# Optimization experiments

Measured on AMD Instinct MI355X. Metric: run time of the kernel, lower is better.

Reference implementation:

```python
import jax, jax.numpy as jnp
import numpy as np

B, P, F, H, NF, E, V, L = 128, 196, 2048, 512, 512, 512, 10000, 20
T = L - 1
EPS = 1e-5  # BatchNorm eps (eval mode, running_mean=0, running_var=1)


def setup_inputs() -> dict:
    key = jax.random.key(0)
    ks = jax.random.split(key, 16)

    def kaiming(k, out_d, in_d):
        return jax.random.normal(k, (out_d, in_d), jnp.float32) * np.float32(np.sqrt(2.0 / in_d))

    encoder_feat = jax.random.normal(ks[0], (B, P, F), jnp.float32)
    gt_captions = jax.random.randint(ks[1], (B, L), 0, V)
    # lengths in [2, L], sorted descending (torch code assumes this), max forced to L
    captions_len = jnp.sort(jax.random.randint(ks[2], (B,), 2, L + 1))[::-1].at[0].set(L)

    emb = jax.random.uniform(ks[3], (V, E), jnp.float32, -0.1, 0.1)
    Wfa = kaiming(ks[4], NF, F); bfa = jnp.zeros((NF,), jnp.float32)
    Wha = kaiming(ks[5], NF, H); bha = jnp.zeros((NF,), jnp.float32)
    Wv = kaiming(ks[6], 1, NF); bv = jnp.zeros((1,), jnp.float32)
    Wh0 = kaiming(ks[7], H, F); bh0 = jnp.zeros((H,), jnp.float32)
    Wc0 = kaiming(ks[8], H, F); bc0 = jnp.zeros((H,), jnp.float32)
    gamma_h = jnp.ones((H,), jnp.float32); beta_h = jnp.zeros((H,), jnp.float32)
    gamma_c = jnp.ones((H,), jnp.float32); beta_c = jnp.zeros((H,), jnp.float32)
    Wfb = kaiming(ks[9], F, H); bfb = jnp.zeros((F,), jnp.float32)
    s = np.float32(1.0 / np.sqrt(H))  # torch LSTMCell default init range
    Wih = jax.random.uniform(ks[10], (4 * H, E + F), jnp.float32, -s, s)
    Whh = jax.random.uniform(ks[11], (4 * H, H), jnp.float32, -s, s)
    bih = jax.random.uniform(ks[12], (4 * H,), jnp.float32, -s, s)
    bhh = jax.random.uniform(ks[13], (4 * H,), jnp.float32, -s, s)
    Wfc = kaiming(ks[14], V, H); bfc = jnp.zeros((V,), jnp.float32)

    return dict(encoder_feat=encoder_feat, emb=emb, Wfa=Wfa, bfa=bfa, Wha=Wha, bha=bha,
                Wv=Wv, bv=bv, Wh0=Wh0, bh0=bh0, Wc0=Wc0, bc0=bc0,
                gamma_h=gamma_h, beta_h=beta_h, gamma_c=gamma_c, beta_c=beta_c,
                Wfb=Wfb, bfb=bfb, Wih=Wih, Whh=Whh, bih=bih, bhh=bhh,
                Wfc=Wfc, bfc=bfc, gt_captions=gt_captions, captions_len=captions_len)


def reference(encoder_feat, emb, Wfa, bfa, Wha, bha, Wv, bv, Wh0, bh0, Wc0, bc0,
              gamma_h, beta_h, gamma_c, beta_c, Wfb, bfb, Wih, Whh, bih, bhh,
              Wfc, bfc, gt_captions, captions_len):
    # Eval-mode semantics: dropout = identity, weight-drop inactive,
    # BatchNorm1d uses default running stats (mean=0, var=1).
    def bn(x, g, b):
        return g * (x / jnp.sqrt(1.0 + EPS)) + b

    feat = encoder_feat.mean(axis=1)                       # [B, F]
    h = bn(jax.nn.sigmoid(feat @ Wh0.T + bh0), gamma_h, beta_h)
    c = bn(jax.nn.sigmoid(feat @ Wc0.T + bc0), gamma_c, beta_c)

    # attention key projection is h-independent: hoist out of the time loop
    feat_att = jnp.einsum('bpf,nf->bpn', encoder_feat, Wfa) + bfa  # [B, P, NF]
    emb_seq = emb[gt_captions]                                      # [B, L, E]

    # ragged batch handled by masking (equivalent to torch's [:batch_size_t] slicing)
    mask = (jnp.arange(T)[:, None] < (captions_len - 1)[None, :]).astype(encoder_feat.dtype)  # [T, B]
    xs = (jnp.swapaxes(emb_seq[:, :T], 0, 1), mask)

    def step(carry, xt):
        h, c = carry
        emb_t, m = xt                                      # [B, E], [B]
        att = jax.nn.relu(feat_att + (h @ Wha.T + bha)[:, None, :])
        e = jnp.einsum('bpn,n->bp', att, Wv[0]) + bv[0]    # [B, P]
        alpha = jax.nn.softmax(e, axis=1)
        context = jnp.einsum('bpf,bp->bf', encoder_feat, alpha)
        gate = jax.nn.sigmoid(h @ Wfb.T + bfb)             # [B, F]
        x = jnp.concatenate([emb_t, gate * context], axis=1)
        gates = x @ Wih.T + bih + h @ Whh.T + bhh          # [B, 4H]
        i, f, g, o = jnp.split(gates, 4, axis=1)
        c_new = jax.nn.sigmoid(f) * c + jax.nn.sigmoid(i) * jnp.tanh(g)
        h_new = jax.nn.sigmoid(o) * jnp.tanh(c_new)
        preds = h_new @ Wfc.T + bfc                        # [B, V]
        mf = m[:, None]
        return (h_new, c_new), (preds * mf, alpha * mf)

    _, (preds, alphas) = jax.lax.scan(step, (h, c), xs)
    predictions = jnp.swapaxes(preds, 0, 1)                # [B, T, V]
    alphas = jnp.swapaxes(alphas, 0, 1)                    # [B, T, P]
    return predictions, alphas
```

## Files before the change

kernel.cpp:

```cpp
#include <hip/hip_runtime.h>
#include <cstdint>
#include <cstddef>

#define B_  128
#define P_  196
#define F_  2048
#define H_  512
#define NF_ 512
#define E_  512
#define V_  10000
#define L_  20
#define T_  19
#define NPAD_ 10112

typedef short s8v __attribute__((ext_vector_type(8)));
typedef float f32x4 __attribute__((ext_vector_type(4)));
typedef unsigned short u16x8 __attribute__((ext_vector_type(8)));

__device__ __forceinline__ float sigf(float x) { return 1.0f / (1.0f + expf(-x)); }
__device__ __forceinline__ ushort f2b(float f) {
    unsigned u = __builtin_bit_cast(unsigned, f);
    u += 0x7fff + ((u >> 16) & 1);
    return (ushort)(u >> 16);
}
__device__ __forceinline__ float b2f(ushort h) {
    unsigned u = ((unsigned)h) << 16;
    return __builtin_bit_cast(float, u);
}

__global__ __launch_bounds__(256)
void zero_buf(float4* __restrict__ p, int n16) {
    int i = blockIdx.x * 256 + threadIdx.x;
    if (i < n16) p[i] = make_float4(0.f, 0.f, 0.f, 0.f);
}

__global__ __launch_bounds__(256)
void cast_mat(const float* __restrict__ s, ushort* __restrict__ d,
              long long total, int cols, int sld, int srows) {
    long long i4 = ((long long)blockIdx.x * 256 + threadIdx.x) * 4;
    if (i4 >= total) return;
    int n = (int)(i4 / cols);
    int k = (int)(i4 - (long long)n * cols);
    float4 v = make_float4(0.f, 0.f, 0.f, 0.f);
    if (n < srows) v = *(const float4*)(s + (size_t)n * sld + k);
    ushort4 o;
    o.x = f2b(v.x); o.y = f2b(v.y); o.z = f2b(v.z); o.w = f2b(v.w);
    *(ushort4*)(d + i4) = o;
}

__global__ __launch_bounds__(256)
void cast_perm(const float* __restrict__ s, ushort* __restrict__ d,
               int cols, int sld) {
    int idx = blockIdx.x * 256 + threadIdx.x;
    int i4 = idx * 4;
    int n = i4 / cols;
    int k = i4 - n * cols;
    int r = (n & 3) * H_ + (n >> 2);
    float4 v = *(const float4*)(s + (size_t)r * sld + k);
    ushort4 o;
    o.x = f2b(v.x); o.y = f2b(v.y); o.z = f2b(v.z); o.w = f2b(v.w);
    *(ushort4*)(d + (size_t)n * cols + k) = o;
}

__global__ __launch_bounds__(256)
void build_bg(const float* __restrict__ bih, const float* __restrict__ bhh,
              float* __restrict__ bg) {
    int n = blockIdx.x * 256 + threadIdx.x;
    int r = (n & 3) * H_ + (n >> 2);
    bg[n] = bih[r] + bhh[r];
}

#define NCP_ (2560 + NPAD_)
__global__ __launch_bounds__(256)
void build_bcp(const float* __restrict__ bha, const float* __restrict__ bfb,
               const float* __restrict__ bfc, float* __restrict__ bcp) {
    int n = blockIdx.x * 256 + threadIdx.x;
    if (n >= NCP_) return;
    float v;
    if (n < 512) v = bha[n];
    else if (n < 2560) v = bfb[n - 512];
    else { int r = n - 2560; v = (r < V_) ? bfc[r] : 0.0f; }
    bcp[n] = v;
}

__global__ __launch_bounds__(256)
void mean_cast_kernel(const float* __restrict__ enc, ushort* __restrict__ encb,
                      float* __restrict__ feat) {
    int b = blockIdx.x >> 3;
    int f = ((blockIdx.x & 7) << 8) + threadIdx.x;
    const float* p = enc + (size_t)b * P_ * F_ + f;
    ushort* pb = encb + (size_t)b * P_ * F_ + f;
    float s = 0.0f;
    for (int q = 0; q < P_; q++) {
        float v = p[(size_t)q * F_];
        pb[(size_t)q * F_] = f2b(v);
        s += v;
    }
    feat[b * F_ + f] = s * (1.0f / 196.0f);
}

__global__ __launch_bounds__(256) void mean_kernel(const float* __restrict__ enc,
                                                   float* __restrict__ feat) {
    int b = blockIdx.x >> 3;
    int f = ((blockIdx.x & 7) << 8) + threadIdx.x;
    const float* p = enc + (size_t)b * P_ * F_ + f;
    float s = 0.0f;
    for (int q = 0; q < P_; q++) s += p[(size_t)q * F_];
    feat[b * F_ + f] = s * (1.0f / 196.0f);
}

__global__ __launch_bounds__(256) void gather_b(const float* __restrict__ emb,
                                                const int* __restrict__ gt,
                                                ushort* __restrict__ embx) {
    int idx = blockIdx.x * 256 + threadIdx.x;
    int i4 = idx * 4;
    int e = i4 & (E_ - 1);
    int bt = i4 >> 9;
    int b = bt / T_, t = bt - b * T_;
    int tok = gt[b * L_ + t];
    float4 v = *(const float4*)(emb + (size_t)tok * E_ + e);
    ushort4 o;
    o.x = f2b(v.x); o.y = f2b(v.y); o.z = f2b(v.z); o.w = f2b(v.w);
    *(ushort4*)(embx + i4) = o;
}

__global__ __launch_bounds__(256)
void gemm_biasb(const float* __restrict__ A, int lda,
                const float* __restrict__ W, int ldw,
                const float* __restrict__ bias,
                ushort* __restrict__ C, long long ldc,
                int M, int N, int K) {
    __shared__ float As[16][65];
    __shared__ float Ws[16][65];
    const int tid = threadIdx.x;
    const int m0 = blockIdx.y << 6;
    const int n0 = blockIdx.x << 6;
    const int row = tid >> 2;
    const int kq  = (tid & 3) << 2;
    const int ty = tid >> 4, tx = tid & 15;
    float acc[4][4] = {};
    for (int k0 = 0; k0 < K; k0 += 16) {
        float4 av = make_float4(0.f, 0.f, 0.f, 0.f);
        float4 wv = make_float4(0.f, 0.f, 0.f, 0.f);
        int m = m0 + row;
        if (m < M) av = *(const float4*)(A + (size_t)m * lda + k0 + kq);
        int n = n0 + row;
        if (n < N) wv = *(const float4*)(W + (size_t)n * ldw + k0 + kq);
        __syncthreads();
        As[kq + 0][row] = av.x; As[kq + 1][row] = av.y;
        As[kq + 2][row] = av.z; As[kq + 3][row] = av.w;
        Ws[kq + 0][row] = wv.x; Ws[kq + 1][row] = wv.y;
        Ws[kq + 2][row] = wv.z; Ws[kq + 3][row] = wv.w;
        __syncthreads();
#pragma unroll
        for (int k = 0; k < 16; k++) {
            float a[4], w[4];
#pragma unroll
            for (int i = 0; i < 4; i++) a[i] = As[k][(ty << 2) + i];
#pragma unroll
            for (int j = 0; j < 4; j++) w[j] = Ws[k][(tx << 2) + j];
#pragma unroll
            for (int i = 0; i < 4; i++)
#pragma unroll
                for (int j = 0; j < 4; j++)
                    acc[i][j] = fmaf(a[i], w[j], acc[i][j]);
        }
    }
#pragma unroll
    for (int i = 0; i < 4; i++) {
        int m = m0 + (ty << 2) + i;
        if (m >= M) continue;
#pragma unroll
        for (int j = 0; j < 4; j++) {
            int n = n0 + (tx << 2) + j;
            if (n >= N) continue;
            C[(size_t)m * ldc + n] = f2b(acc[i][j] + bias[n]);
        }
    }
}

enum { MEPI_NONE = 0, MEPI_BIAS = 1, MEPI_BIASB = 2, MEPI_PREDS = 3 };

__device__ __forceinline__ void stage_tile(const ushort* __restrict__ g, int ld,
                                           int row0, int k0, ushort* lds,
                                           int rows, int w, int l) {
    int nchunk = rows >> 4;
    for (int c = w; c < nchunk; c += 4) {
        int flat = c * 1024 + l * 16;
        int r = flat >> 6;
        int ce = (flat & 63) >> 1;
        const ushort* gp = g + (size_t)(row0 + r) * ld + (k0 + ce);
        __builtin_amdgcn_global_load_lds(
            (const __attribute__((address_space(1))) void*)gp,
            (__attribute__((address_space(3))) void*)(lds + c * 512),
            16, 0, 0);
    }
}

template <int BM, int EPI, int DUAL, int SWZ = 0, int MSK = 0>
__global__ __launch_bounds__(256)
void mfma_gemm(const ushort* __restrict__ A1, int lda1,
               const ushort* __restrict__ W1, int ldw1, int K1,
               const ushort* __restrict__ A2, int lda2,
               const ushort* __restrict__ W2, int ldw2, int K2,
               const float* __restrict__ bias, void* __restrict__ Cout, long long ldc,
               void* __restrict__ Cout2,
               int M, int N,
               const int* __restrict__ clen, int tcur) {
    __shared__ ushort As[BM * 32];
    __shared__ ushort Bs[128 * 32];
    const int tid = threadIdx.x;
    const int w = tid >> 6, l = tid & 63;
    const int wr = w >> 1, wc = w & 1;
    constexpr int WM = BM / 2;
    constexpr int AF = WM / 16;
    int bx = blockIdx.x, by = blockIdx.y;
    if (SWZ) {
        const int gx = gridDim.x;
        const int nwg = gx * gridDim.y;
        const int fid = by * gx + bx;
        const int q = nwg >> 3, r = nwg & 7;
        const int xcd = fid & 7, idx = fid >> 3;
        const int nf = (xcd < r ? xcd * (q + 1)
                                : r * (q + 1) + (xcd - r) * q) + idx;
        bx = nf % gx; by = nf / gx;
    }
    if (MSK) {
        int cl = clen[by * BM + (l & (BM - 1))];
        if (!__any(tcur < cl - 1)) return;
    }
    const int m0 = by * BM;
    const int n0 = bx * 128;
    const int lrow = l & 15, lk8 = (l >> 4) * 8;
    const int kz = blockIdx.z, nzz = gridDim.z;

    f32x4 acc[AF][4] = {};

    for (int pass = 0; pass < 1 + DUAL; pass++) {
        const ushort* A = pass ? A2 : A1;
        const ushort* W = pass ? W2 : W1;
        const int lda = pass ? lda2 : lda1;
        const int ldw = pass ? ldw2 : ldw1;
        const int K  = pass ? K2 : K1;
        const int chunk = K / nzz;
        const int kbeg = kz * chunk;
        const int kend = kbeg + chunk;
        for (int k0 = kbeg; k0 < kend; k0 += 32) {
            __syncthreads();
            stage_tile(A, lda, m0, k0, As, BM, w, l);
            stage_tile(W, ldw, n0, k0, Bs, 128, w, l);
            __syncthreads();
            s8v af[AF], bf[4];
#pragma unroll
            for (int i = 0; i < AF; i++)
                af[i] = *(const s8v*)(As + (wr * WM + i * 16 + lrow) * 32 + lk8);
#pragma unroll
            for (int j = 0; j < 4; j++)
                bf[j] = *(const s8v*)(Bs + (wc * 64 + j * 16 + lrow) * 32 + lk8);
#pragma unroll
            for (int i = 0; i < AF; i++)
#pragma unroll
                for (int j = 0; j < 4; j++)
                    acc[i][j] = __builtin_amdgcn_mfma_f32_16x16x32_bf16(
                        af[i], bf[j], acc[i][j], 0, 0, 0);
        }
    }

    float* Cz = (float*)Cout + (size_t)kz * (size_t)M * ldc;
#pragma unroll
    for (int i = 0; i < AF; i++) {
        int rb = m0 + wr * WM + i * 16 + (l >> 4) * 4;
#pragma unroll
        for (int j = 0; j < 4; j++) {
            int n = n0 + wc * 64 + j * 16 + (l & 15);
            if (n >= N) continue;
#pragma unroll
            for (int r = 0; r < 4; r++) {
                int m = rb + r;
                float v = acc[i][j][r];
                if (EPI == MEPI_NONE) {
                    Cz[(size_t)m * ldc + n] = v;
                } else if (EPI == MEPI_BIAS) {
                    ((float*)Cout)[(size_t)m * ldc + n] = v + bias[n];
                } else if (EPI == MEPI_BIASB) {
                    ((ushort*)Cout)[(size_t)m * ldc + n] = f2b(v + bias[n]);
                } else if (EPI == MEPI_PREDS) {
                    if (n < V_) {
                        int bb = m & (B_ - 1);
                        int tt = m >> 7;
                        float mk = (tt < clen[bb] - 1) ? 1.0f : 0.0f;
                        ((float*)Cout)[((size_t)bb * T_ + tt) * (size_t)V_ + n] =
                            (v + bias[n]) * mk;
                    }
                }
            }
        }
    }
}

__global__ __launch_bounds__(256)
void h0c0_final(const float* __restrict__ part,
                const float* __restrict__ b0,
                const float* __restrict__ g0,
                const float* __restrict__ bt0,
                float* __restrict__ cbuf, ushort* __restrict__ hb) {
    int idx = blockIdx.x * 256 + threadIdx.x;
    int b = idx >> 9, j = idx & 511;
    const float rbn = 1.0f / sqrtf(1.0f + 1e-5f);
    float sh = b0[j], sc = b0[j + 512];
    for (int z = 0; z < 4; z++) {
        sh += part[((size_t)z * B_ + b) * 1024 + j];
        sc += part[((size_t)z * B_ + b) * 1024 + j + 512];
    }
    float hv = g0[j] * (sigf(sh) * rbn) + bt0[j];
    float cv = g0[j + 512] * (sigf(sc) * rbn) + bt0[j + 512];
    cbuf[idx] = cv;
    hb[idx] = f2b(hv);
}

template <int BF>
__global__ __launch_bounds__(256)
void attn_ctx(const void* __restrict__ encv, const ushort* __restrict__ fa,
              const float* __restrict__ combo, const float* __restrict__ Wv,
              float* __restrict__ alphas_out, const int* __restrict__ clen,
              ushort* __restrict__ gctxb, int t) {
    int b = blockIdx.x >> 1;
    if (t >= clen[b] - 1) return;
    int half = blockIdx.x & 1;
    int tid = threadIdx.x;
    int w = tid >> 6, l = tid & 63;
    __shared__ float eS[256];
    __shared__ float red[256];
    __shared__ float pc[128 * 8];
    const float* hap = combo + (size_t)b * 2560;
    float ha8[8], wv8[8];
#pragma unroll
    for (int i = 0; i < 8; i++) { ha8[i] = hap[l * 8 + i]; wv8[i] = Wv[l * 8 + i]; }
    eS[tid] = -1e30f;
    __syncthreads();
    const ushort* fab = fa + (size_t)b * P_ * NF_;
    for (int p = w; p < P_; p += 4) {
        const ushort* fp = fab + (size_t)p * NF_ + l * 8;
        ushort4 u0 = *(const ushort4*)fp;
        ushort4 u1 = *(const ushort4*)(fp + 4);
        float s = 0.0f, v;
        v = b2f(u0.x) + ha8[0]; v = v > 0.f ? v : 0.f; s = fmaf(v, wv8[0], s);
        v = b2f(u0.y) + ha8[1]; v = v > 0.f ? v : 0.f; s = fmaf(v, wv8[1], s);
        v = b2f(u0.z) + ha8[2]; v = v > 0.f ? v : 0.f; s = fmaf(v, wv8[2], s);
        v = b2f(u0.w) + ha8[3]; v = v > 0.f ? v : 0.f; s = fmaf(v, wv8[3], s);
        v = b2f(u1.x) + ha8[4]; v = v > 0.f ? v : 0.f; s = fmaf(v, wv8[4], s);
        v = b2f(u1.y) + ha8[5]; v = v > 0.f ? v : 0.f; s = fmaf(v, wv8[5], s);
        v = b2f(u1.z) + ha8[6]; v = v > 0.f ? v : 0.f; s = fmaf(v, wv8[6], s);
        v = b2f(u1.w) + ha8[7]; v = v > 0.f ? v : 0.f; s = fmaf(v, wv8[7], s);
#pragma unroll
        for (int off = 32; off > 0; off >>= 1) s += __shfl_down(s, off, 64);
        if (l == 0) eS[p] = s;
    }
    __syncthreads();
    float ev = eS[tid];
    red[tid] = ev;
    __syncthreads();
    for (int s = 128; s > 0; s >>= 1) {
        if (tid < s) red[tid] = fmaxf(red[tid], red[tid + s]);
        __syncthreads();
    }
    float mx = red[0];
    __syncthreads();
    float ex = expf(ev - mx);
    red[tid] = ex;
    __syncthreads();
    for (int s = 128; s > 0; s >>= 1) {
        if (tid < s) red[tid] += red[tid + s];
        __syncthreads();
    }
    float inv = 1.0f / red[0];
    float a = ex * inv;
    __syncthreads();
    eS[tid] = a;
    if (half == 0 && tid < P_) {
        alphas_out[((size_t)b * T_ + t) * P_ + tid] = a;
    }
    __syncthreads();

    int tl = tid & 127;
    int pr = tid >> 7;
    int pp0 = pr * 98;
    int f0 = (half << 10) + tl * 8;
    float s[8] = {};
    if (BF) {
        const ushort* ep = (const ushort*)encv + (size_t)b * P_ * F_ +
                           (size_t)pp0 * F_ + f0;
        for (int p = 0; p < 98; p++) {
            u16x8 u = *(const u16x8*)(ep + (size_t)p * F_);
            float al = eS[pp0 + p];
#pragma unroll
            for (int i = 0; i < 8; i++) s[i] = fmaf(al, b2f(u[i]), s[i]);
        }
    } else {
        const float* ep = (const float*)encv + (size_t)b * P_ * F_ +
                          (size_t)pp0 * F_ + f0;
        for (int p = 0; p < 98; p++) {
            float4 u0 = *(const float4*)(ep + (size_t)p * F_);
            float4 u1 = *(const float4*)(ep + (size_t)p * F_ + 4);
            float al = eS[pp0 + p];
            s[0] = fmaf(al, u0.x, s[0]); s[1] = fmaf(al, u0.y, s[1]);
            s[2] = fmaf(al, u0.z, s[2]); s[3] = fmaf(al, u0.w, s[3]);
            s[4] = fmaf(al, u1.x, s[4]); s[5] = fmaf(al, u1.y, s[5]);
            s[6] = fmaf(al, u1.z, s[6]); s[7] = fmaf(al, u1.w, s[7]);
        }
    }
    if (pr) {
#pragma unroll
        for (int i = 0; i < 8; i++) pc[tl * 8 + i] = s[i];
    }
    __syncthreads();
    if (!pr) {
        const float* gp = combo + (size_t)b * 2560 + 512 + f0;
        float4 ga = *(const float4*)gp;
        float4 gb = *(const float4*)(gp + 4);
        float gv[8] = {ga.x, ga.y, ga.z, ga.w, gb.x, gb.y, gb.z, gb.w};
        ushort o[8];
#pragma unroll
        for (int i = 0; i < 8; i++)
            o[i] = f2b(sigf(gv[i]) * (s[i] + pc[tl * 8 + i]));
        *(u16x8*)(gctxb + (size_t)b * F_ + f0) = *(u16x8*)o;
    }
}

__global__ __launch_bounds__(256)
void lstm_perm(const float* __restrict__ gatesP,
               const float* __restrict__ embprojP,
               const float* __restrict__ bg,
               const int* __restrict__ clen,
               float* __restrict__ cbuf, ushort* __restrict__ hout, int t) {
    int idx = blockIdx.x * 256 + threadIdx.x;
    int b = idx >> 9, j = idx & (H_ - 1);
    if (t >= clen[b] - 1) return;
    int n0 = j * 4;
    float4 g = *(const float4*)(embprojP + ((size_t)b * T_ + t) * 2048 + n0);
    float4 bgv = *(const float4*)(bg + n0);
    g.x += bgv.x; g.y += bgv.y; g.z += bgv.z; g.w += bgv.w;
#pragma unroll
    for (int z = 0; z < 4; z++) {
        float4 p = *(const float4*)(gatesP + ((size_t)z * B_ + b) * 2048 + n0);
        g.x += p.x; g.y += p.y; g.z += p.z; g.w += p.w;
    }
    float cn = sigf(g.y) * cbuf[idx] + sigf(g.x) * tanhf(g.z);
    float hn = sigf(g.w) * tanhf(cn);
    cbuf[idx] = cn;
    hout[idx] = f2b(hn);
}

extern "C" void kernel_launch(void* const* d_in, const int* in_sizes, int n_in,
                              void* d_out, int out_size, void* d_ws, size_t ws_size,
                              hipStream_t stream) {
    const float* enc = (const float*)d_in[0];
    const float* emb = (const float*)d_in[1];
    const float* Wfa = (const float*)d_in[2];
    const float* bfa = (const float*)d_in[3];
    const float* Wha = (const float*)d_in[4];
    const float* bha = (const float*)d_in[5];
    const float* Wv  = (const float*)d_in[6];
    const float* Wh0 = (const float*)d_in[8];
    const float* bh0 = (const float*)d_in[9];
    const float* Wc0 = (const float*)d_in[10];
    const float* bc0 = (const float*)d_in[11];
    const float* gh  = (const float*)d_in[12];
    const float* bth = (const float*)d_in[13];
    const float* gc  = (const float*)d_in[14];
    const float* btc = (const float*)d_in[15];
    const float* Wfb = (const float*)d_in[16];
    const float* bfb = (const float*)d_in[17];
    const float* Wih = (const float*)d_in[18];
    const float* Whh = (const float*)d_in[19];
    const float* bih = (const float*)d_in[20];
    const float* bhh = (const float*)d_in[21];
    const float* Wfc = (const float*)d_in[22];
    const float* bfc = (const float*)d_in[23];
    const int* gt   = (const int*)d_in[24];
    const int* clen = (const int*)d_in[25];

    float* out_pred  = (float*)d_out;
    float* out_alpha = out_pred + (size_t)B_ * T_ * V_;

    char* wp = (char*)d_ws;
    auto alloc = [&](size_t bytes) {
        char* p = wp;
        wp += (bytes + 255) & ~(size_t)255;
        return p;
    };
    float*  feat     = (float*)alloc((size_t)B_ * F_ * 4);
    float*  cbuf     = (float*)alloc((size_t)B_ * H_ * 4);
    float*  combo    = (float*)alloc((size_t)B_ * 2560 * 4);
    float*  embprojP = (float*)alloc((size_t)B_ * T_ * 2048 * 4);
    float*  gatesP   = (float*)alloc((size_t)4 * B_ * 2048 * 4);
    float*  hcpart   = (float*)alloc((size_t)4 * B_ * 1024 * 4);
    float*  bcp      = (float*)alloc((size_t)NCP_ * 4);
    float*  bg       = (float*)alloc(2048 * 4);
    float*  b0comb   = (float*)alloc(1024 * 4);
    float*  g0comb   = (float*)alloc(1024 * 4);
    float*  bt0comb  = (float*)alloc(1024 * 4);
    ushort* hall     = (ushort*)alloc((size_t)(T_ + 1) * B_ * H_ * 2);
    ushort* gctxb    = (ushort*)alloc((size_t)B_ * F_ * 2);
    ushort* embxb    = (ushort*)alloc((size_t)B_ * T_ * E_ * 2);
    ushort* fattb    = (ushort*)alloc((size_t)B_ * P_ * NF_ * 2);
    ushort* featb    = (ushort*)alloc((size_t)B_ * F_ * 2);
    ushort* Wfab     = (ushort*)alloc((size_t)NF_ * F_ * 2);
    ushort* WihEbP   = (ushort*)alloc((size_t)2048 * E_ * 2);
    ushort* WihFbP   = (ushort*)alloc((size_t)2048 * F_ * 2);
    ushort* WhhbP    = (ushort*)alloc((size_t)2048 * H_ * 2);
    ushort* Wcp      = (ushort*)alloc((size_t)NCP_ * H_ * 2);
    ushort* W0comb   = (ushort*)alloc((size_t)1024 * F_ * 2);
    ushort* encb     = (ushort*)alloc((size_t)B_ * P_ * F_ * 2);
    const bool big = ((size_t)(wp - (char*)d_ws) <= ws_size);

    auto castM = [&](const float* s, ushort* d, long long rows, int cols, int sld, int srows) {
        long long total = rows * (long long)cols;
        cast_mat<<<(int)((total + 1023) / 1024), 256, 0, stream>>>(s, d, total, cols, sld, srows);
    };

    {
        int n16h = (int)(((size_t)(T_ + 1) * B_ * H_ * 2) / 16);
        zero_buf<<<(n16h + 255) / 256, 256, 0, stream>>>((float4*)hall, n16h);
        int n16a = (int)(((size_t)B_ * T_ * P_ * 4) / 16);
        zero_buf<<<(n16a + 255) / 256, 256, 0, stream>>>((float4*)out_alpha, n16a);
    }

    castM(Wfa, Wfab, NF_, F_, F_, NF_);
    cast_perm<<<(2048 * E_) / 1024, 256, 0, stream>>>(Wih, WihEbP, E_, E_ + F_);
    cast_perm<<<(2048 * F_) / 1024, 256, 0, stream>>>(Wih + E_, WihFbP, F_, E_ + F_);
    cast_perm<<<(2048 * H_) / 1024, 256, 0, stream>>>(Whh, WhhbP, H_, H_);
    castM(Wha, Wcp, NF_, H_, H_, NF_);
    castM(Wfb, Wcp + (size_t)512 * H_, F_, H_, H_, F_);
    castM(Wfc, Wcp + (size_t)2560 * H_, NPAD_, H_, H_, V_);
    castM(Wh0, W0comb, H_, F_, F_, H_);
    castM(Wc0, W0comb + (size_t)H_ * F_, H_, F_, F_, H_);
    build_bg<<<2048 / 256, 256, 0, stream>>>(bih, bhh, bg);
    build_bcp<<<(NCP_ + 255) / 256, 256, 0, stream>>>(bha, bfb, bfc, bcp);
    hipMemcpyAsync(b0comb, bh0, H_ * 4, hipMemcpyDeviceToDevice, stream);
    hipMemcpyAsync(b0comb + H_, bc0, H_ * 4, hipMemcpyDeviceToDevice, stream);
    hipMemcpyAsync(g0comb, gh, H_ * 4, hipMemcpyDeviceToDevice, stream);
    hipMemcpyAsync(g0comb + H_, gc, H_ * 4, hipMemcpyDeviceToDevice, stream);
    hipMemcpyAsync(bt0comb, bth, H_ * 4, hipMemcpyDeviceToDevice, stream);
    hipMemcpyAsync(bt0comb + H_, btc, H_ * 4, hipMemcpyDeviceToDevice, stream);

    if (big) mean_cast_kernel<<<B_ * 8, 256, 0, stream>>>(enc, encb, feat);
    else     mean_kernel<<<B_ * 8, 256, 0, stream>>>(enc, feat);
    castM(feat, featb, B_, F_, F_, B_);
    mfma_gemm<32, MEPI_NONE, 0><<<dim3(1024 / 128, B_ / 32, 4), 256, 0, stream>>>(
        featb, F_, W0comb, F_, F_, nullptr, 0, nullptr, 0, 0,
        nullptr, hcpart, 1024, nullptr, B_, 1024, nullptr, 0);
    h0c0_final<<<(B_ * H_) / 256, 256, 0, stream>>>(hcpart, b0comb, g0comb, bt0comb, cbuf, hall);
    gather_b<<<(B_ * T_ * E_) / 1024, 256, 0, stream>>>(emb, gt, embxb);

    if (big) {
        mfma_gemm<128, MEPI_BIASB, 0, 1><<<dim3(NF_ / 128, (B_ * P_) / 128, 1), 256, 0, stream>>>(
            encb, F_, Wfab, F_, F_, nullptr, 0, nullptr, 0, 0,
            bfa, fattb, NF_, nullptr, B_ * P_, NF_, nullptr, 0);
    } else {
        gemm_biasb<<<dim3(NF_ / 64, (B_ * P_) / 64), 256, 0, stream>>>(
            enc, F_, Wfa, F_, bfa, fattb, NF_, B_ * P_, NF_, F_);
    }
    mfma_gemm<128, MEPI_NONE, 0><<<dim3(2048 / 128, (B_ * T_) / 128, 1), 256, 0, stream>>>(
        embxb, E_, WihEbP, E_, E_, nullptr, 0, nullptr, 0, 0,
        nullptr, embprojP, 2048, nullptr, B_ * T_, 2048, nullptr, 0);

    mfma_gemm<32, MEPI_BIAS, 0><<<dim3(2560 / 128, B_ / 32, 1), 256, 0, stream>>>(
        hall, H_, Wcp, H_, H_, nullptr, 0, nullptr, 0, 0,
        bcp, combo, 2560, nullptr, B_, 2560, nullptr, 0);

    for (int t = 0; t < T_; t++) {
        ushort* hin  = hall + (size_t)t * B_ * H_;
        ushort* hout = hall + (size_t)(t + 1) * B_ * H_;
        if (big) attn_ctx<1><<<B_ * 2, 256, 0, stream>>>(encb, fattb, combo, Wv,
                                                         out_alpha, clen, gctxb, t);
        else     attn_ctx<0><<<B_ * 2, 256, 0, stream>>>(enc, fattb, combo, Wv,
                                                         out_alpha, clen, gctxb, t);
        mfma_gemm<32, MEPI_NONE, 1, 0, 1><<<dim3(2048 / 128, B_ / 32, 4), 256, 0, stream>>>(
            gctxb, F_, WihFbP, F_, F_, hin, H_, WhhbP, H_, H_,
            nullptr, gatesP, 2048, nullptr, B_, 2048, clen, t);
        lstm_perm<<<(B_ * H_) / 256, 256, 0, stream>>>(
            gatesP, embprojP, bg, clen, cbuf, hout, t);
        mfma_gemm<32, MEPI_BIAS, 0, 0, 1><<<dim3(2560 / 128, B_ / 32, 1), 256, 0, stream>>>(
            hout, H_, Wcp, H_, H_, nullptr, 0, nullptr, 0, 0,
            bcp, combo, 2560, nullptr, B_, 2560, clen, t + 1);
    }

    mfma_gemm<128, MEPI_PREDS, 0, 1><<<dim3(NPAD_ / 128, (B_ * T_) / 128, 1), 256, 0, stream>>>(
        hall + (size_t)B_ * H_, H_, Wcp + (size_t)2560 * H_, H_, H_,
        nullptr, 0, nullptr, 0, 0,
        bcp + 2560, out_pred, V_, nullptr, B_ * T_, NPAD_, clen, 0);
}
```

Before: 1.918 ms.

## Fuse per-timestep scan kernels into one persistent kernel with grid barriers

Replaces the per-timestep launches (attention/context, gates GEMM, LSTM cell, combo GEMM) with one persistent 256-block kernel. Phases are separated by an atomic-counter grid barrier. Because captions are sorted by length, work in each phase is limited to the active batch prefix rather than masked per block. This removes roughly 76 kernel launches and their gaps. In exchange it adds spin-barrier cost, caps occupancy at the persistent grid, and depends on all blocks being co-resident; the spin loop also gives up after a bounded count, which could silently break ordering.

Measured after the change: 3.224 ms. +68.1%, slower.

```diff
diff --git a/kernel.cpp b/kernel.cpp
--- a/kernel.cpp
+++ b/kernel.cpp
@@ -12,6 +12,8 @@
 #define L_  20
 #define T_  19
 #define NPAD_ 10112
+#define BH_ (B_ * H_)
+#define NBLK_ 256
 
 typedef short s8v __attribute__((ext_vector_type(8)));
 typedef float f32x4 __attribute__((ext_vector_type(4)));
@@ -26,6 +28,21 @@
 __device__ __forceinline__ float b2f(ushort h) {
     unsigned u = ((unsigned)h) << 16;
     return __builtin_bit_cast(float, u);
+}
+
+__device__ __forceinline__ void gbar(unsigned* cnt, unsigned target) {
+    __syncthreads();
+    if (threadIdx.x == 0) {
+        __threadfence();
+        atomicAdd(cnt, 1u);
+        int spins = 0;
+        while (atomicAdd(cnt, 0u) < target && spins < (1 << 20)) {
+            __builtin_amdgcn_s_sleep(2);
+            ++spins;
+        }
+        __threadfence();
+    }
+    __syncthreads();
 }
 
 __global__ __launch_bounds__(256)
@@ -197,7 +214,7 @@
     }
 }
 
-template <int BM, int EPI, int DUAL, int SWZ = 0, int MSK = 0>
+template <int BM, int EPI, int DUAL, int SWZ = 0>
 __global__ __launch_bounds__(256)
 void mfma_gemm(const ushort* __restrict__ A1, int lda1,
                const ushort* __restrict__ W1, int ldw1, int K1,
@@ -225,10 +242,6 @@
                                 : r * (q + 1) + (xcd - r) * q) + idx;
         bx = nf % gx; by = nf / gx;
     }
-    if (MSK) {
-        int cl = clen[by * BM + (l & (BM - 1))];
-        if (!__any(tcur < cl - 1)) return;
-    }
     const int m0 = by * BM;
     const int n0 = bx * 128;
     const int lrow = l & 15, lk8 = (l >> 4) * 8;
@@ -318,27 +331,122 @@
     hb[idx] = f2b(hv);
 }
 
+
+struct ScanArgs {
+    const void* encv;
+    const ushort* fattb;
+    float* combo;
+    const float* Wv;
+    float* out_alpha;
+    const int* clen;
+    ushort* gctxb;
+    const ushort* WihF;
+    const ushort* Whh;
+    float* gatesP;
+    const float* embprojP;
+    const float* bg;
+    float* cbuf;
+    ushort* hall;
+    const ushort* Wcp;
+    const float* bcp;
+    unsigned* bar;
+};
+
+__device__ __forceinline__ void combo_unit(float* smem, const ushort* hsrc,
+                                           const ushort* Wcp, const float* bcp,
+                                           float* combo, int u, int tid) {
+    ushort* As = (ushort*)smem;
+    ushort* Bs = (ushort*)smem + 1024;
+    const int w = tid >> 6, l = tid & 63;
+    const int wr = w >> 1, wc = w & 1;
+    const int lrow = l & 15, lk8 = (l >> 4) * 8;
+    const int bx = u % 20, by = u / 20;
+    const int m0 = by * 32, n0 = bx * 128;
+    f32x4 acc[4] = {};
+    for (int k0 = 0; k0 < 512; k0 += 32) {
+        __syncthreads();
+        stage_tile(hsrc, 512, m0, k0, As, 32, w, l);
+        stage_tile(Wcp, 512, n0, k0, Bs, 128, w, l);
+        __syncthreads();
+        s8v af = *(const s8v*)(As + (wr * 16 + lrow) * 32 + lk8);
+        s8v bf[4];
+#pragma unroll
+        for (int j = 0; j < 4; j++)
+            bf[j] = *(const s8v*)(Bs + (wc * 64 + j * 16 + lrow) * 32 + lk8);
+#pragma unroll
+        for (int j = 0; j < 4; j++)
+            acc[j] = __builtin_amdgcn_mfma_f32_16x16x32_bf16(af, bf[j], acc[j], 0, 0, 0);
+    }
+    const int rb = m0 + wr * 16 + (l >> 4) * 4;
+#pragma unroll
+    for (int j = 0; j < 4; j++) {
+        int n = n0 + wc * 64 + j * 16 + (l & 15);
+#pragma unroll
+        for (int r = 0; r < 4; r++)
+            combo[(size_t)(rb + r) * 2560 + n] = acc[j][r] + bcp[n];
+    }
+}
+
+__device__ __forceinline__ void gates_unit(float* smem, const ushort* gctxb,
+                                           const ushort* WihF, const ushort* hin,
+                                           const ushort* Whh, float* gatesP,
+                                           int u, int nyb, int tid) {
+    ushort* As = (ushort*)smem;
+    ushort* Bs = (ushort*)smem + 1024;
+    const int w = tid >> 6, l = tid & 63;
+    const int wr = w >> 1, wc = w & 1;
+    const int lrow = l & 15, lk8 = (l >> 4) * 8;
+    const int bx = u & 15;
+    const int rem = u >> 4;
+    const int by = rem % nyb, kz = rem / nyb;
+    const int m0 = by * 32, n0 = bx * 128;
+    f32x4 acc[4] = {};
+#pragma unroll
+    for (int pass = 0; pass < 2; pass++) {
+        const ushort* A = pass ? hin : gctxb;
+        const ushort* W = pass ? Whh : WihF;
+        const int ld = pass ? 512 : 2048;
+        const int chunk = (pass ? 512 : 2048) >> 2;
+        const int kbeg = kz * chunk;
+        for (int k0 = kbeg; k0 < kbeg + chunk; k0 += 32) {
+            __syncthreads();
+            stage_tile(A, ld, m0, k0, As, 32, w, l);
+            stage_tile(W, ld, n0, k0, Bs, 128, w, l);
+            __syncthreads();
+            s8v af = *(const s8v*)(As + (wr * 16 + lrow) * 32 + lk8);
+            s8v bf[4];
+#pragma unroll
+            for (int j = 0; j < 4; j++)
+                bf[j] = *(const s8v*)(Bs + (wc * 64 + j * 16 + lrow) * 32 + lk8);
+#pragma unroll
+            for (int j = 0; j < 4; j++)
+                acc[j] = __builtin_amdgcn_mfma_f32_16x16x32_bf16(af, bf[j], acc[j], 0, 0, 0);
+        }
+    }
+    const int rb = m0 + wr * 16 + (l >> 4) * 4;
+#pragma unroll
+    for (int j = 0; j < 4; j++) {
+        int n = n0 + wc * 64 + j * 16 + (l & 15);
+#pragma unroll
+        for (int r = 0; r < 4; r++)
+            gatesP[((size_t)kz * B_ + (rb + r)) * 2048 + n] = acc[j][r];
+    }
+}
+
 template <int BF>
-__global__ __launch_bounds__(256)
-void attn_ctx(const void* __restrict__ encv, const ushort* __restrict__ fa,
-              const float* __restrict__ combo, const float* __restrict__ Wv,
-              float* __restrict__ alphas_out, const int* __restrict__ clen,
-              ushort* __restrict__ gctxb, int t) {
-    int b = blockIdx.x >> 1;
-    if (t >= clen[b] - 1) return;
-    int half = blockIdx.x & 1;
-    int tid = threadIdx.x;
-    int w = tid >> 6, l = tid & 63;
-    __shared__ float eS[256];
-    __shared__ float red[256];
-    __shared__ float pc[128 * 8];
-    const float* hap = combo + (size_t)b * 2560;
+__device__ __forceinline__ void attn_unit(float* smem, const ScanArgs& a,
+                                          int t, int b, int half, int tid) {
+    float* eS  = smem;
+    float* red = smem + 256;
+    float* pc  = smem + 512;
+    const int w = tid >> 6, l = tid & 63;
+    const float* hap = a.combo + (size_t)b * 2560;
     float ha8[8], wv8[8];
 #pragma unroll
-    for (int i = 0; i < 8; i++) { ha8[i] = hap[l * 8 + i]; wv8[i] = Wv[l * 8 + i]; }
+    for (int i = 0; i < 8; i++) { ha8[i] = hap[l * 8 + i]; wv8[i] = a.Wv[l * 8 + i]; }
     eS[tid] = -1e30f;
     __syncthreads();
-    const ushort* fab = fa + (size_t)b * P_ * NF_;
+    const ushort* fab = a.fattb + (size_t)b * P_ * NF_;
     for (int p = w; p < P_; p += 4) {
         const ushort* fp = fab + (size_t)p * NF_ + l * 8;
         ushort4 u0 = *(const ushort4*)fp;
@@ -374,11 +482,11 @@
         __syncthreads();
     }
     float inv = 1.0f / red[0];
-    float a = ex * inv;
-    __syncthreads();
-    eS[tid] = a;
+    float aa = ex * inv;
+    __syncthreads();
+    eS[tid] = aa;
     if (half == 0 && tid < P_) {
-        alphas_out[((size_t)b * T_ + t) * P_ + tid] = a;
+        a.out_alpha[((size_t)b * T_ + t) * P_ + tid] = aa;
     }
     __syncthreads();
 
@@ -388,7 +496,7 @@
     int f0 = (half << 10) + tl * 8;
     float s[8] = {};
     if (BF) {
-        const ushort* ep = (const ushort*)encv + (size_t)b * P_ * F_ +
+        const ushort* ep = (const ushort*)a.encv + (size_t)b * P_ * F_ +
                            (size_t)pp0 * F_ + f0;
         for (int p = 0; p < 98; p++) {
             u16x8 u = *(const u16x8*)(ep + (size_t)p * F_);
@@ -397,7 +505,7 @@
             for (int i = 0; i < 8; i++) s[i] = fmaf(al, b2f(u[i]), s[i]);
         }
     } else {
-        const float* ep = (const float*)encv + (size_t)b * P_ * F_ +
+        const float* ep = (const float*)a.encv + (size_t)b * P_ * F_ +
                           (size_t)pp0 * F_ + f0;
         for (int p = 0; p < 98; p++) {
             float4 u0 = *(const float4*)(ep + (size_t)p * F_);
@@ -415,7 +523,7 @@
     }
     __syncthreads();
     if (!pr) {
-        const float* gp = combo + (size_t)b * 2560 + 512 + f0;
+        const float* gp = a.combo + (size_t)b * 2560 + 512 + f0;
         float4 ga = *(const float4*)gp;
         float4 gb = *(const float4*)(gp + 4);
         float gv[8] = {ga.x, ga.y, ga.z, ga.w, gb.x, gb.y, gb.z, gb.w};
@@ -423,32 +531,67 @@
 #pragma unroll
         for (int i = 0; i < 8; i++)
             o[i] = f2b(sigf(gv[i]) * (s[i] + pc[tl * 8 + i]));
-        *(u16x8*)(gctxb + (size_t)b * F_ + f0) = *(u16x8*)o;
-    }
-}
-
-__global__ __launch_bounds__(256)
-void lstm_perm(const float* __restrict__ gatesP,
-               const float* __restrict__ embprojP,
-               const float* __restrict__ bg,
-               const int* __restrict__ clen,
-               float* __restrict__ cbuf, ushort* __restrict__ hout, int t) {
-    int idx = blockIdx.x * 256 + threadIdx.x;
-    int b = idx >> 9, j = idx & (H_ - 1);
-    if (t >= clen[b] - 1) return;
-    int n0 = j * 4;
-    float4 g = *(const float4*)(embprojP + ((size_t)b * T_ + t) * 2048 + n0);
-    float4 bgv = *(const float4*)(bg + n0);
-    g.x += bgv.x; g.y += bgv.y; g.z += bgv.z; g.w += bgv.w;
-#pragma unroll
-    for (int z = 0; z < 4; z++) {
-        float4 p = *(const float4*)(gatesP + ((size_t)z * B_ + b) * 2048 + n0);
-        g.x += p.x; g.y += p.y; g.z += p.z; g.w += p.w;
-    }
-    float cn = sigf(g.y) * cbuf[idx] + sigf(g.x) * tanhf(g.z);
-    float hn = sigf(g.w) * tanhf(cn);
-    cbuf[idx] = cn;
-    hout[idx] = f2b(hn);
+        *(u16x8*)(a.gctxb + (size_t)b * F_ + f0) = *(u16x8*)o;
+    }
+    __syncthreads();
+}
+
+template <int BF>
+__global__ __launch_bounds__(256, 2)
+void scan_mega(ScanArgs a) {
+    const int bid = blockIdx.x;
+    const int tid = threadIdx.x;
+    const int l = tid & 63;
+    __shared__ __align__(16) float smem[2560];
+    const int cl1 = a.clen[l] - 1;
+    const int cl2 = a.clen[64 + l] - 1;
+    unsigned tgt = 0;
+
+    for (int u = bid; u < 80; u += NBLK_)
+        combo_unit(smem, a.hall, a.Wcp, a.bcp, a.combo, u, tid);
+
+    for (int t = 0; t < T_; t++) {
+        unsigned long long m1 = __ballot(t < cl1);
+        unsigned long long m2 = __ballot(t < cl2);
+        const int na = __popcll(m1) + __popcll(m2);
+        const int nyb = (na + 31) >> 5;
+
+        tgt += NBLK_; gbar(a.bar, tgt);
+        for (int u = bid; u < 2 * na; u += NBLK_)
+            attn_unit<BF>(smem, a, t, u >> 1, u & 1, tid);
+        tgt += NBLK_; gbar(a.bar, tgt);
+        for (int u = bid; u < 16 * nyb * 4; u += NBLK_)
+            gates_unit(smem, a.gctxb, a.WihF, a.hall + (size_t)t * BH_,
+                       a.Whh, a.gatesP, u, nyb, tid);
+        tgt += NBLK_; gbar(a.bar, tgt);
+        for (int u = bid; u < 2 * na; u += NBLK_) {
+            int idx = u * 256 + tid;
+            int b = idx >> 9, j = idx & (H_ - 1);
+            int n0 = j * 4;
+            float4 g = *(const float4*)(a.embprojP + ((size_t)b * T_ + t) * 2048 + n0);
+            float4 bgv = *(const float4*)(a.bg + n0);
+            g.x += bgv.x; g.y += bgv.y; g.z += bgv.z; g.w += bgv.w;
+#pragma unroll
+            for (int z = 0; z < 4; z++) {
+                float4 p = *(const float4*)(a.gatesP + ((size_t)z * B_ + b) * 2048 + n0);
+                g.x += p.x; g.y += p.y; g.z += p.z; g.w += p.w;
+            }
+            float cn = sigf(g.y) * a.cbuf[idx] + sigf(g.x) * tanhf(g.z);
+            float hn = sigf(g.w) * tanhf(cn);
+            a.cbuf[idx] = cn;
+            (a.hall + (size_t)(t + 1) * BH_)[idx] = f2b(hn);
+        }
+        if (t + 1 < T_) {
+            tgt += NBLK_; gbar(a.bar, tgt);
+            unsigned long long n1 = __ballot(t + 1 < cl1);
+            unsigned long long n2 = __ballot(t + 1 < cl2);
+            const int na2 = __popcll(n1) + __popcll(n2);
+            const int nyb2 = (na2 + 31) >> 5;
+            for (int u = bid; u < 20 * nyb2; u += NBLK_)
+                combo_unit(smem, a.hall + (size_t)(t + 1) * BH_, a.Wcp, a.bcp,
+                           a.combo, u, tid);
+        }
+    }
 }
 
 extern "C" void kernel_launch(void* const* d_in, const int* in_sizes, int n_in,
@@ -500,6 +643,7 @@
     float*  b0comb   = (float*)alloc(1024 * 4);
     float*  g0comb   = (float*)alloc(1024 * 4);
     float*  bt0comb  = (float*)alloc(1024 * 4);
+    unsigned* barbuf = (unsigned*)alloc(256);
     ushort* hall     = (ushort*)alloc((size_t)(T_ + 1) * B_ * H_ * 2);
     ushort* gctxb    = (ushort*)alloc((size_t)B_ * F_ * 2);
     ushort* embxb    = (ushort*)alloc((size_t)B_ * T_ * E_ * 2);
@@ -524,6 +668,7 @@
         zero_buf<<<(n16h + 255) / 256, 256, 0, stream>>>((float4*)hall, n16h);
         int n16a = (int)(((size_t)B_ * T_ * P_ * 4) / 16);
         zero_buf<<<(n16a + 255) / 256, 256, 0, stream>>>((float4*)out_alpha, n16a);
+        zero_buf<<<1, 256, 0, stream>>>((float4*)barbuf, 16);
     }
 
     castM(Wfa, Wfab, NF_, F_, F_, NF_);
@@ -565,25 +710,27 @@
         embxb, E_, WihEbP, E_, E_, nullptr, 0, nullptr, 0, 0,
         nullptr, embprojP, 2048, nullptr, B_ * T_, 2048, nullptr, 0);
 
-    mfma_gemm<32, MEPI_BIAS, 0><<<dim3(2560 / 128, B_ / 32, 1), 256, 0, stream>>>(
-        hall, H_, Wcp, H_, H_, nullptr, 0, nullptr, 0, 0,
-        bcp, combo, 2560, nullptr, B_, 2560, nullptr, 0);
-
-    for (int t = 0; t < T_; t++) {
-        ushort* hin  = hall + (size_t)t * B_ * H_;
-        ushort* hout = hall + (size_t)(t + 1) * B_ * H_;
-        if (big) attn_ctx<1><<<B_ * 2, 256, 0, stream>>>(encb, fattb, combo, Wv,
-                                                         out_alpha, clen, gctxb, t);
-        else     attn_ctx<0><<<B_ * 2, 256, 0, stream>>>(enc, fattb, combo, Wv,
-                                                         out_alpha, clen, gctxb, t);
-        mfma_gemm<32, MEPI_NONE, 1, 0, 1><<<dim3(2048 / 128, B_ / 32, 4), 256, 0, stream>>>(
-            gctxb, F_, WihFbP, F_, F_, hin, H_, WhhbP, H_, H_,
-            nullptr, gatesP, 2048, nullptr, B_, 2048, clen, t);
-        lstm_perm<<<(B_ * H_) / 256, 256, 0, stream>>>(
-            gatesP, embprojP, bg, clen, cbuf, hout, t);
-        mfma_gemm<32, MEPI_BIAS, 0, 0, 1><<<dim3(2560 / 128, B_ / 32, 1), 256, 0, stream>>>(
-            hout, H_, Wcp, H_, H_, nullptr, 0, nullptr, 0, 0,
-            bcp, combo, 2560, nullptr, B_, 2560, clen, t + 1);
+    {
+        ScanArgs sa;
+        sa.encv = big ? (const void*)encb : (const void*)enc;
+        sa.fattb = fattb;
+        sa.combo = combo;
+        sa.Wv = Wv;
+        sa.out_alpha = out_alpha;
+        sa.clen = clen;
+        sa.gctxb = gctxb;
+        sa.WihF = WihFbP;
+        sa.Whh = WhhbP;
+        sa.gatesP = gatesP;
+        sa.embprojP = embprojP;
+        sa.bg = bg;
+        sa.cbuf = cbuf;
+        sa.hall = hall;
+        sa.Wcp = Wcp;
+        sa.bcp = bcp;
+        sa.bar = barbuf;
+        if (big) scan_mega<1><<<NBLK_, 256, 0, stream>>>(sa);
+        else     scan_mega<0><<<NBLK_, 256, 0, stream>>>(sa);
     }
 
     mfma_gemm<128, MEPI_PREDS, 0, 1><<<dim3(NPAD_ / 128, (B_ * T_) / 128, 1), 256, 0, stream>>>(
```
